# Optimization experiments

Measured on AMD Instinct MI355X. Metric: run time of the kernel, lower is better.

Reference implementation:

```python
import jax, jax.numpy as jnp
import numpy as np

EMBED_DIM = 768
N_HEADS = 12
TIME_RATIO = 0.5
HEAD_DIM = EMBED_DIM // N_HEADS          # 64
T_HEAD = int(HEAD_DIM * TIME_RATIO)      # 32 time dims per head
T_DIM = T_HEAD * N_HEADS                 # 384 time dims overall
EPS = 1e-5


def _ln(v, g, b):
    m = jnp.mean(v, axis=-1, keepdims=True)
    var = jnp.mean((v - m) ** 2, axis=-1, keepdims=True)
    return (v - m) * jax.lax.rsqrt(var + EPS) * g + b


def minkowski_ln(x, g_t, b_t, g_s, b_s):
    # normalize time-like and space-like channel groups separately
    xt, xs = x[..., :T_DIM], x[..., T_DIM:]
    return jnp.concatenate([_ln(xt, g_t, b_t), _ln(xs, g_s, b_s)], axis=-1)


def lorentz_attention(x, Wq, bq, Wk, bk, Wv, bv, Wo, bo):
    B, S, D = x.shape
    def heads(W, b):
        return (x @ W + b).reshape(B, S, N_HEADS, HEAD_DIM).transpose(0, 2, 1, 3)
    q, k, v = heads(Wq, bq), heads(Wk, bk), heads(Wv, bv)
    # Minkowski metric signature (-,...,-,+,...,+) within each head
    eta = jnp.concatenate([-jnp.ones((T_HEAD,), x.dtype), jnp.ones((HEAD_DIM - T_HEAD,), x.dtype)])
    logits = jnp.einsum('bhqd,bhkd->bhqk', q * eta, k) / np.sqrt(HEAD_DIM).astype(np.float32)
    attn = jax.nn.softmax(logits, axis=-1)
    o = jnp.einsum('bhqk,bhkd->bhqd', attn, v)
    o = o.transpose(0, 2, 1, 3).reshape(B, S, D)
    return o @ Wo + bo


def setup_inputs() -> dict:
    key = jax.random.key(0)
    ks = jax.random.split(key, 16)
    D, H4 = EMBED_DIM, EMBED_DIM * 4
    s = 0.02
    inp = {
        'x': jax.random.normal(ks[0], (2, 2048, D), jnp.float32),
        'Wq': jax.random.normal(ks[1], (D, D), jnp.float32) * s, 'bq': jnp.zeros((D,), jnp.float32),
        'Wk': jax.random.normal(ks[2], (D, D), jnp.float32) * s, 'bk': jnp.zeros((D,), jnp.float32),
        'Wv': jax.random.normal(ks[3], (D, D), jnp.float32) * s, 'bv': jnp.zeros((D,), jnp.float32),
        'Wo': jax.random.normal(ks[4], (D, D), jnp.float32) * s, 'bo': jnp.zeros((D,), jnp.float32),
        'g1t': jnp.ones((T_DIM,), jnp.float32), 'b1t': jnp.zeros((T_DIM,), jnp.float32),
        'g1s': jnp.ones((D - T_DIM,), jnp.float32), 'b1s': jnp.zeros((D - T_DIM,), jnp.float32),
        'W1': jax.random.normal(ks[5], (D, H4), jnp.float32) * s, 'bb1': jnp.zeros((H4,), jnp.float32),
        'W2': jax.random.normal(ks[6], (H4, D), jnp.float32) * s, 'bb2': jnp.zeros((D,), jnp.float32),
        'g2t': jnp.ones((T_DIM,), jnp.float32), 'b2t': jnp.zeros((T_DIM,), jnp.float32),
        'g2s': jnp.ones((D - T_DIM,), jnp.float32), 'b2s': jnp.zeros((D - T_DIM,), jnp.float32),
    }
    return inp


def reference(x, Wq, bq, Wk, bk, Wv, bv, Wo, bo,
              g1t, b1t, g1s, b1s, W1, bb1, W2, bb2,
              g2t, b2t, g2s, b2s):
    a = lorentz_attention(x, Wq, bq, Wk, bk, Wv, bv, Wo, bo)
    x = minkowski_ln(x + a, g1t, b1t, g1s, b1s)
    h = jax.nn.gelu(x @ W1 + bb1) @ W2 + bb2
    x = minkowski_ln(x + h, g2t, b2t, g2s, b2s)
    return x
```

## Files before the change

### kernel.cpp

```cpp
#include <hip/hip_runtime.h>
#include <cstddef>
#include <cstdint>

#define D_EMB  768
#define NHEAD  12
#define HDIM   64
#define THEAD  32
#define SEQ    2048
#define BATCH  2
#define NROW   (BATCH*SEQ)
#define HID4   3072

typedef unsigned short u16;
typedef __bf16 bf16x8 __attribute__((ext_vector_type(8)));
typedef float  f32x4  __attribute__((ext_vector_type(4)));
typedef unsigned short u16x8 __attribute__((ext_vector_type(8)));

__device__ __forceinline__ u16 f2bf(float f) {
    unsigned u = __builtin_bit_cast(unsigned, f);
    return (u16)((u + 0x7FFFu + ((u >> 16) & 1u)) >> 16);
}
__device__ __forceinline__ float bf2f(u16 h) {
    return __builtin_bit_cast(float, (unsigned)h << 16);
}

__device__ __forceinline__ void gload_lds16(const void* g, void* l) {
    __builtin_amdgcn_global_load_lds(
        reinterpret_cast<const __attribute__((address_space(1))) void*>(
            reinterpret_cast<uintptr_t>(g)),
        reinterpret_cast<__attribute__((address_space(3))) void*>(
            (uint32_t)reinterpret_cast<uintptr_t>(l)),
        16, 0, 0);
}

__device__ __forceinline__ void tcast(float (*t)[33], const float* __restrict__ W,
                                      u16* __restrict__ WT, int K, int M,
                                      int mt, int kt)
{
    const int m0 = mt * 32, k0 = kt * 32;
    const int tx = threadIdx.x & 31, ty = threadIdx.x >> 5;
#pragma unroll
    for (int i = 0; i < 32; i += 8)
        t[ty + i][tx] = W[(size_t)(k0 + ty + i) * M + m0 + tx];
    __syncthreads();
#pragma unroll
    for (int i = 0; i < 32; i += 8)
        WT[(size_t)(m0 + ty + i) * K + k0 + tx] = f2bf(t[tx][ty + i]);
}

__global__ __launch_bounds__(256)
void prep(const float* __restrict__ Wq, const float* __restrict__ Wk,
          const float* __restrict__ Wv, const float* __restrict__ Wo,
          const float* __restrict__ W1, const float* __restrict__ W2,
          const float* __restrict__ bq, const float* __restrict__ bk,
          const float* __restrict__ bv, const float* __restrict__ x,
          u16* __restrict__ WqkvoT, u16* __restrict__ W1T,
          u16* __restrict__ W2T, u16* __restrict__ xb,
          float* __restrict__ bqkv)
{
    __shared__ float t[32][33];
    const int bid = blockIdx.x;
    if (bid < 2304) {
        const int z = bid / 576, r = bid % 576;
        const float* W = z == 0 ? Wq : z == 1 ? Wk : z == 2 ? Wv : Wo;
        tcast(t, W, WqkvoT + (size_t)z * 768 * 768, 768, 768, r % 24, r / 24);
    } else if (bid < 4608) {
        const int r = bid - 2304;
        tcast(t, W1, W1T, 768, 3072, r % 96, r / 96);
    } else if (bid < 6912) {
        const int r = bid - 4608;
        tcast(t, W2, W2T, 3072, 768, r % 24, r / 24);
    } else if (bid < 8448) {
        const int i = (bid - 6912) * 2048 + threadIdx.x * 8;
        const float4 a = *reinterpret_cast<const float4*>(x + i);
        const float4 b = *reinterpret_cast<const float4*>(x + i + 4);
        u16x8 h;
        h[0] = f2bf(a.x); h[1] = f2bf(a.y); h[2] = f2bf(a.z); h[3] = f2bf(a.w);
        h[4] = f2bf(b.x); h[5] = f2bf(b.y); h[6] = f2bf(b.z); h[7] = f2bf(b.w);
        *reinterpret_cast<u16x8*>(xb + i) = h;
    } else {
        const int i = (bid - 8448) * 256 + threadIdx.x;
        if (i < 2304)
            bqkv[i] = i < 768 ? bq[i] : (i < 1536 ? bk[i - 768] : bv[i - 1536]);
    }
}

template<int EPI>
__global__ __launch_bounds__(256)
void gemm_bf16(const u16* __restrict__ A, const u16* __restrict__ B,
               const float* __restrict__ bias, void* __restrict__ Cp,
               u16* __restrict__ VTp, int K, int N)
{
    __shared__ u16 As[2][128 * 32];
    __shared__ u16 Bs[2][128 * 32];
    const int tid  = threadIdx.x;
    const int lane = tid & 63;
    const int w    = tid >> 6;
    const int m0 = blockIdx.x * 128, n0 = blockIdx.y * 128;
    const int wr = (w >> 1) << 6, wc = (w & 1) << 6;

    const int seg0 = (w << 11) + lane * 16;
    const int row0 = seg0 >> 6, cb0 = (seg0 & 63) >> 1;
    const int seg1 = seg0 + 1024;
    const int row1 = seg1 >> 6, cb1 = (seg1 & 63) >> 1;
    const u16* a0 = A + (size_t)(m0 + row0) * K + cb0;
    const u16* a1 = A + (size_t)(m0 + row1) * K + cb1;
    const u16* b0 = B + (size_t)(n0 + row0) * K + cb0;
    const u16* b1 = B + (size_t)(n0 + row1) * K + cb1;
    const int lo0 = (w * 2 + 0) << 9;
    const int lo1 = (w * 2 + 1) << 9;

    int aIdx[4], bIdx[4];
#pragma unroll
    for (int i = 0; i < 4; ++i) {
        aIdx[i] = (wr + i * 16 + (lane & 15)) * 32 + ((lane >> 4) << 3);
        bIdx[i] = (wc + i * 16 + (lane & 15)) * 32 + ((lane >> 4) << 3);
    }

    f32x4 acc[4][4];
#pragma unroll
    for (int i = 0; i < 4; ++i)
#pragma unroll
        for (int j = 0; j < 4; ++j)
#pragma unroll
            for (int q = 0; q < 4; ++q) acc[i][j][q] = 0.f;

    gload_lds16(a0, &As[0][lo0]);
    gload_lds16(a1, &As[0][lo1]);
    gload_lds16(b0, &Bs[0][lo0]);
    gload_lds16(b1, &Bs[0][lo1]);
    __syncthreads();

    int cur = 0;
    for (int k0 = 0; k0 < K; k0 += 32) {
        if (k0 + 32 < K) {
            gload_lds16(a0 + k0 + 32, &As[cur ^ 1][lo0]);
            gload_lds16(a1 + k0 + 32, &As[cur ^ 1][lo1]);
            gload_lds16(b0 + k0 + 32, &Bs[cur ^ 1][lo0]);
            gload_lds16(b1 + k0 + 32, &Bs[cur ^ 1][lo1]);
        }
        bf16x8 af[4], bv[4];
#pragma unroll
        for (int i = 0; i < 4; ++i)
            af[i] = *reinterpret_cast<const bf16x8*>(&As[cur][aIdx[i]]);
#pragma unroll
        for (int j = 0; j < 4; ++j)
            bv[j] = *reinterpret_cast<const bf16x8*>(&Bs[cur][bIdx[j]]);
#pragma unroll
        for (int i = 0; i < 4; ++i)
#pragma unroll
            for (int j = 0; j < 4; ++j)
                acc[i][j] = __builtin_amdgcn_mfma_f32_16x16x32_bf16(
                    af[i], bv[j], acc[i][j], 0, 0, 0);
        __syncthreads();
        cur ^= 1;
    }

#pragma unroll
    for (int i = 0; i < 4; ++i) {
#pragma unroll
        for (int q = 0; q < 4; ++q) {
            const int row = m0 + wr + i * 16 + ((lane >> 4) << 2) + q;
#pragma unroll
            for (int j = 0; j < 4; ++j) {
                const int col = n0 + wc + j * 16 + (lane & 15);
                float v = acc[i][j][q] + bias[col];
                if (EPI == 2) {
                    const float u3 = v * v * v;
                    v = 0.5f * v * (1.f + tanhf(0.7978845608028654f *
                                                (v + 0.044715f * u3)));
                    ((u16*)Cp)[(size_t)row * N + col] = f2bf(v);
                } else {
                    if (n0 < 1536) {
                        ((u16*)Cp)[(size_t)row * 1536 + col] = f2bf(v);
                    } else {
                        const int c2 = col - 1536;
                        const int hh = c2 >> 6, dd = c2 & 63;
                        const int bb = row >> 11, tok = row & 2047;
                        const int t = tok & 63;
                        const int p = ((t & 15) << 2) | (t >> 4);
                        VTp[((size_t)(bb * NHEAD + hh) * HDIM + dd) * SEQ
                            + (tok & ~63) + p] = f2bf(v);
                    }
                }
            }
        }
    }
}

__global__ __launch_bounds__(256)
void gemm_n64(const u16* __restrict__ A, const u16* __restrict__ B,
              const float* __restrict__ bias, float* __restrict__ C,
              int K, int N)
{
    __shared__ u16 As[2][64 * 32];
    __shared__ u16 Bs[2][128 * 32];
    const int tid  = threadIdx.x;
    const int lane = tid & 63;
    const int w    = tid >> 6;
    const int l15  = lane & 15;
    const int g    = lane >> 4;
    const int m0 = blockIdx.x * 64, n0 = blockIdx.y * 128;

    const int segA = (w << 10) + lane * 16;
    const int rowA = segA >> 6, cbA = (segA & 63) >> 1;
    const u16* aP = A + (size_t)(m0 + rowA) * K + cbA;
    const int loA = w << 9;
    const int seg0 = (w << 11) + lane * 16;
    const int row0 = seg0 >> 6, cb0 = (seg0 & 63) >> 1;
    const int seg1 = seg0 + 1024;
    const int row1 = seg1 >> 6, cb1 = (seg1 & 63) >> 1;
    const u16* b0 = B + (size_t)(n0 + row0) * K + cb0;
    const u16* b1 = B + (size_t)(n0 + row1) * K + cb1;
    const int lo0 = w << 10, lo1 = (w << 10) + 512;

    int aIdx[4], bIdx[2];
#pragma unroll
    for (int i = 0; i < 4; ++i) aIdx[i] = (i * 16 + l15) * 32 + (g << 3);
#pragma unroll
    for (int j = 0; j < 2; ++j) bIdx[j] = ((w << 5) + j * 16 + l15) * 32 + (g << 3);

    f32x4 acc[4][2];
#pragma unroll
    for (int i = 0; i < 4; ++i)
#pragma unroll
        for (int j = 0; j < 2; ++j)
#pragma unroll
            for (int q = 0; q < 4; ++q) acc[i][j][q] = 0.f;

    gload_lds16(aP, &As[0][loA]);
    gload_lds16(b0, &Bs[0][lo0]);
    gload_lds16(b1, &Bs[0][lo1]);
    __syncthreads();

    int cur = 0;
    for (int k0 = 0; k0 < K; k0 += 32) {
        if (k0 + 32 < K) {
            gload_lds16(aP + k0 + 32, &As[cur ^ 1][loA]);
            gload_lds16(b0 + k0 + 32, &Bs[cur ^ 1][lo0]);
            gload_lds16(b1 + k0 + 32, &Bs[cur ^ 1][lo1]);
        }
        bf16x8 af[4], bv[2];
#pragma unroll
        for (int i = 0; i < 4; ++i)
            af[i] = *reinterpret_cast<const bf16x8*>(&As[cur][aIdx[i]]);
#pragma unroll
        for (int j = 0; j < 2; ++j)
            bv[j] = *reinterpret_cast<const bf16x8*>(&Bs[cur][bIdx[j]]);
#pragma unroll
        for (int i = 0; i < 4; ++i)
#pragma unroll
            for (int j = 0; j < 2; ++j)
                acc[i][j] = __builtin_amdgcn_mfma_f32_16x16x32_bf16(
                    af[i], bv[j], acc[i][j], 0, 0, 0);
        __syncthreads();
        cur ^= 1;
    }

#pragma unroll
    for (int i = 0; i < 4; ++i) {
#pragma unroll
        for (int q = 0; q < 4; ++q) {
            const int row = m0 + i * 16 + (g << 2) + q;
#pragma unroll
            for (int j = 0; j < 2; ++j) {
                const int col = n0 + (w << 5) + j * 16 + l15;
                C[(size_t)row * N + col] = acc[i][j][q] + bias[col];
            }
        }
    }
}

#define SM_SCALE 0.18033688011112042f

__global__ __launch_bounds__(256)
void attn_mfma(const u16* __restrict__ QK, const u16* __restrict__ VT,
               u16* __restrict__ O)
{
    __shared__ u16 Ks[2][64 * 64];
    __shared__ u16 Vs[2][64 * 64];
    __shared__ u16 Ps[64 * 72];

    const int tid  = threadIdx.x;
    const int lane = tid & 63;
    const int w    = tid >> 6;
    const int l15  = lane & 15;
    const int g    = lane >> 4;
    const int bh   = blockIdx.x;
    const int b    = bh / NHEAD, h = bh % NHEAD;
    const int q0   = blockIdx.y * 64;
    const int bS   = b * SEQ;

    bf16x8 aq[2];
    {
        const u16* Qg = QK + (size_t)(bS + q0 + (w << 4) + l15) * 1536 + h * HDIM;
#pragma unroll
        for (int kk = 0; kk < 2; ++kk) {
            const u16x8 hq = *reinterpret_cast<const u16x8*>(Qg + kk * 32 + g * 8);
            const float sc = (kk == 0) ? -SM_SCALE : SM_SCALE;
            u16x8 hs;
#pragma unroll
            for (int j = 0; j < 8; ++j)
                hs[j] = __builtin_bit_cast(u16, (__bf16)(bf2f(hq[j]) * sc));
            aq[kk] = __builtin_bit_cast(bf16x8, hs);
        }
    }

    const int rl = lane >> 3;
    const int cs = ((lane & 7) ^ rl) << 3;
    const u16* pK = QK + (size_t)(bS + 16 * w + rl) * 1536 + 768 + h * HDIM + cs;
    const u16* pV = VT + ((size_t)(b * NHEAD + h) * HDIM + 16 * w + rl) * SEQ + cs;

    int swz[2];
#pragma unroll
    for (int kk = 0; kk < 2; ++kk)
        swz[kk] = ((kk * 4 + g) ^ (l15 & 7)) << 3;

    bf16x8 vones;
    {
        u16x8 o16;
#pragma unroll
        for (int j = 0; j < 8; ++j) o16[j] = 0x3F80u;
        vones = __builtin_bit_cast(bf16x8, o16);
    }

    f32x4 accO[4];
#pragma unroll
    for (int n = 0; n < 4; ++n)
#pragma unroll
        for (int q = 0; q < 4; ++q) accO[n][q] = 0.f;
    f32x4 accS;
#pragma unroll
    for (int q = 0; q < 4; ++q) accS[q] = 0.f;

#define ATTN_STAGE(c, kt)                                                   \
    do {                                                                    \
        u16* dK = &Ks[c][w * 1024];                                         \
        u16* dV = &Vs[c][w * 1024];                                         \
        gload_lds16(pK + (size_t)(kt) * 1536,       dK);                    \
        gload_lds16(pK + (size_t)((kt) + 8) * 1536, dK + 512);              \
        gload_lds16(pV + (kt),           dV);                               \
        gload_lds16(pV + (kt) + 8 * SEQ, dV + 512);                         \
    } while (0)

    ATTN_STAGE(0, 0);
    __syncthreads();
    int cur = 0;

    for (int kt = 0; kt < SEQ; kt += 64) {
        if (kt + 64 < SEQ) ATTN_STAGE(cur ^ 1, kt + 64);

        f32x4 sac[4];
#pragma unroll
        for (int n = 0; n < 4; ++n) {
#pragma unroll
            for (int q = 0; q < 4; ++q) sac[n][q] = 0.f;
#pragma unroll
            for (int kk = 0; kk < 2; ++kk) {
                const bf16x8 bk = *reinterpret_cast<const bf16x8*>(
                    &Ks[cur][(n * 16 + l15) * 64 + swz[kk]]);
                sac[n] = __builtin_amdgcn_mfma_f32_16x16x32_bf16(
                    aq[kk], bk, sac[n], 0, 0, 0);
            }
        }

#pragma unroll
        for (int r4 = 0; r4 < 4; ++r4) {
            const int prow = (w << 4) + (g << 2) + r4;
            const float sv0 = __builtin_amdgcn_exp2f(sac[0][r4]);
            const float sv1 = __builtin_amdgcn_exp2f(sac[1][r4]);
            const float sv2 = __builtin_amdgcn_exp2f(sac[2][r4]);
            const float sv3 = __builtin_amdgcn_exp2f(sac[3][r4]);
            ushort4 pk4;
            pk4.x = __builtin_bit_cast(u16, (__bf16)sv0);
            pk4.y = __builtin_bit_cast(u16, (__bf16)sv1);
            pk4.z = __builtin_bit_cast(u16, (__bf16)sv2);
            pk4.w = __builtin_bit_cast(u16, (__bf16)sv3);
            *reinterpret_cast<ushort4*>(&Ps[prow * 72 + (l15 << 2)]) = pk4;
        }

        bf16x8 pa[2];
#pragma unroll
        for (int kk = 0; kk < 2; ++kk)
            pa[kk] = *reinterpret_cast<const bf16x8*>(
                &Ps[((w << 4) + l15) * 72 + kk * 32 + g * 8]);
#pragma unroll
        for (int n = 0; n < 4; ++n) {
#pragma unroll
            for (int kk = 0; kk < 2; ++kk) {
                const bf16x8 bv = *reinterpret_cast<const bf16x8*>(
                    &Vs[cur][(n * 16 + l15) * 64 + swz[kk]]);
                accO[n] = __builtin_amdgcn_mfma_f32_16x16x32_bf16(
                    pa[kk], bv, accO[n], 0, 0, 0);
            }
        }
#pragma unroll
        for (int kk = 0; kk < 2; ++kk)
            accS = __builtin_amdgcn_mfma_f32_16x16x32_bf16(
                pa[kk], vones, accS, 0, 0, 0);
        __syncthreads();
        cur ^= 1;
    }

#pragma unroll
    for (int r4 = 0; r4 < 4; ++r4) {
        const float inv = 1.f / accS[r4];
        const int qr = q0 + (w << 4) + (g << 2) + r4;
#pragma unroll
        for (int n = 0; n < 4; ++n)
            O[(size_t)(bS + qr) * D_EMB + h * HDIM + n * 16 + l15]
                = f2bf(accO[n][r4] * inv);
    }
#undef ATTN_STAGE
}

__global__ __launch_bounds__(256)
void mink_ln(const float* __restrict__ X, const float* __restrict__ R,
             const float* __restrict__ gt, const float* __restrict__ bt,
             const float* __restrict__ gs, const float* __restrict__ bs,
             float* __restrict__ Out, u16* __restrict__ OutB, int nrows)
{
    const int wid  = (int)((blockIdx.x * 256 + threadIdx.x) >> 6);
    const int lane = threadIdx.x & 63;
    const int row  = wid >> 1, half = wid & 1;
    if (row >= nrows) return;

    const float* g  = half ? gs : gt;
    const float* bb = half ? bs : bt;
    const size_t base = (size_t)row * D_EMB + half * 384;

    float v[6];
    float sum = 0.f;
#pragma unroll
    for (int i = 0; i < 6; ++i) {
        const float t = X[base + i * 64 + lane] + R[base + i * 64 + lane];
        v[i] = t; sum += t;
    }
#pragma unroll
    for (int off = 32; off; off >>= 1) sum += __shfl_xor(sum, off);
    const float mean = sum * (1.f / 384.f);

    float ss = 0.f;
#pragma unroll
    for (int i = 0; i < 6; ++i) { const float d = v[i] - mean; ss += d * d; }
#pragma unroll
    for (int off = 32; off; off >>= 1) ss += __shfl_xor(ss, off);
    const float rstd = rsqrtf(ss * (1.f / 384.f) + 1e-5f);

#pragma unroll
    for (int i = 0; i < 6; ++i) {
        const int e = i * 64 + lane;
        const float o = (v[i] - mean) * rstd * g[e] + bb[e];
        Out[base + e] = o;
        if (OutB) OutB[base + e] = f2bf(o);
    }
}

extern "C" void kernel_launch(void* const* d_in, const int* in_sizes, int n_in,
                              void* d_out, int out_size, void* d_ws, size_t ws_size,
                              hipStream_t stream)
{
    const float* x   = (const float*)d_in[0];
    const float* Wq  = (const float*)d_in[1];
    const float* bq  = (const float*)d_in[2];
    const float* Wk  = (const float*)d_in[3];
    const float* bk  = (const float*)d_in[4];
    const float* Wv  = (const float*)d_in[5];
    const float* bv  = (const float*)d_in[6];
    const float* Wo  = (const float*)d_in[7];
    const float* bo  = (const float*)d_in[8];
    const float* g1t = (const float*)d_in[9];
    const float* b1t = (const float*)d_in[10];
    const float* g1s = (const float*)d_in[11];
    const float* b1s = (const float*)d_in[12];
    const float* W1  = (const float*)d_in[13];
    const float* bb1 = (const float*)d_in[14];
    const float* W2  = (const float*)d_in[15];
    const float* bb2 = (const float*)d_in[16];
    const float* g2t = (const float*)d_in[17];
    const float* b2t = (const float*)d_in[18];
    const float* g2s = (const float*)d_in[19];
    const float* b2s = (const float*)d_in[20];
    float* out = (float*)d_out;

    const size_t ND = (size_t)NROW * D_EMB;
    u16* WqkvoT = (u16*)d_ws;
    u16* W1T = WqkvoT + 2359296;
    u16* W2T = W1T + 2359296;
    u16* xb  = W2T + 2359296;
    u16* QKb = xb + ND;
    u16* VTb = QKb + (size_t)NROW * 1536;
    u16* Ab  = VTb + ND;
    u16* Hb  = QKb;
    float* AoF  = (float*)(Ab + ND);
    float* bqkv = AoF;
    float* X1   = AoF + ND;

    const dim3 blk(256);

    prep<<<8457, blk, 0, stream>>>(Wq, Wk, Wv, Wo, W1, W2, bq, bk, bv, x,
                                   WqkvoT, W1T, W2T, xb, bqkv);

    gemm_bf16<3><<<dim3(32, 18), blk, 0, stream>>>(xb, WqkvoT, bqkv, QKb, VTb,
                                                   768, 2304);
    attn_mfma<<<dim3(BATCH * NHEAD, SEQ / 64), blk, 0, stream>>>(QKb, VTb, Ab);

    gemm_n64<<<dim3(64, 6), blk, 0, stream>>>(Ab, WqkvoT + (size_t)2304 * 768,
                                              bo, AoF, 768, 768);
    mink_ln<<<2048, blk, 0, stream>>>(x, AoF, g1t, b1t, g1s, b1s, X1, xb, NROW);
    gemm_bf16<2><<<dim3(32, 24), blk, 0, stream>>>(xb, W1T, bb1, Hb, nullptr,
                                                   768, 3072);
    gemm_n64<<<dim3(64, 6), blk, 0, stream>>>(Hb, W2T, bb2, AoF, 3072, 768);
    mink_ln<<<2048, blk, 0, stream>>>(X1, AoF, g2t, b2t, g2s, b2s, out, nullptr, NROW);
}
```

Measured before the change: 195.1 us.

## Split-K the N=768 GEMMs in two and fold partial sums into LayerNorm

The two output-projection GEMMs (attention out and MLP down) now run with a 2-way split-K over blockIdx.z, doubling the grid from 384 to 768 blocks. The second partial sum is written to a separate fp32 buffer (reusing the QK scratch or the output buffer), and the Minkowski LayerNorm kernels add both partials. The aim is better CU occupancy on a small grid, at the cost of extra fp32 writes and reads. The second LN reads and writes `out` in place, which is safe per element.

```diff
diff --git a/kernel.cpp b/kernel.cpp
--- a/kernel.cpp
+++ b/kernel.cpp
@@ -190,8 +190,8 @@
 
 __global__ __launch_bounds__(256)
 void gemm_n64(const u16* __restrict__ A, const u16* __restrict__ B,
-              const float* __restrict__ bias, float* __restrict__ C,
-              int K, int N)
+              const float* __restrict__ bias, float* __restrict__ C0,
+              float* __restrict__ C1, int Khalf, int Ktot, int N)
 {
     __shared__ u16 As[2][64 * 32];
     __shared__ u16 Bs[2][128 * 32];
@@ -201,17 +201,20 @@
     const int l15  = lane & 15;
     const int g    = lane >> 4;
     const int m0 = blockIdx.x * 64, n0 = blockIdx.y * 128;
+    const int zz = blockIdx.z;
+    const int kbase = zz * Khalf;
+    float* __restrict__ C = zz ? C1 : C0;
 
     const int segA = (w << 10) + lane * 16;
     const int rowA = segA >> 6, cbA = (segA & 63) >> 1;
-    const u16* aP = A + (size_t)(m0 + rowA) * K + cbA;
+    const u16* aP = A + (size_t)(m0 + rowA) * Ktot + kbase + cbA;
     const int loA = w << 9;
     const int seg0 = (w << 11) + lane * 16;
     const int row0 = seg0 >> 6, cb0 = (seg0 & 63) >> 1;
     const int seg1 = seg0 + 1024;
     const int row1 = seg1 >> 6, cb1 = (seg1 & 63) >> 1;
-    const u16* b0 = B + (size_t)(n0 + row0) * K + cb0;
-    const u16* b1 = B + (size_t)(n0 + row1) * K + cb1;
+    const u16* b0 = B + (size_t)(n0 + row0) * Ktot + kbase + cb0;
+    const u16* b1 = B + (size_t)(n0 + row1) * Ktot + kbase + cb1;
     const int lo0 = w << 10, lo1 = (w << 10) + 512;
 
     int aIdx[4], bIdx[2];
@@ -234,8 +237,8 @@
     __syncthreads();
 
     int cur = 0;
-    for (int k0 = 0; k0 < K; k0 += 32) {
-        if (k0 + 32 < K) {
+    for (int k0 = 0; k0 < Khalf; k0 += 32) {
+        if (k0 + 32 < Khalf) {
             gload_lds16(aP + k0 + 32, &As[cur ^ 1][loA]);
             gload_lds16(b0 + k0 + 32, &Bs[cur ^ 1][lo0]);
             gload_lds16(b1 + k0 + 32, &Bs[cur ^ 1][lo1]);
@@ -265,7 +268,8 @@
 #pragma unroll
             for (int j = 0; j < 2; ++j) {
                 const int col = n0 + (w << 5) + j * 16 + l15;
-                C[(size_t)row * N + col] = acc[i][j][q] + bias[col];
+                const float bb = zz ? 0.f : bias[col];
+                C[(size_t)row * N + col] = acc[i][j][q] + bb;
             }
         }
     }
@@ -415,7 +419,8 @@
 }
 
 __global__ __launch_bounds__(256)
-void mink_ln(const float* __restrict__ X, const float* __restrict__ R,
+void mink_ln(const float* __restrict__ X, const float* __restrict__ R1,
+             const float* __restrict__ R2,
              const float* __restrict__ gt, const float* __restrict__ bt,
              const float* __restrict__ gs, const float* __restrict__ bs,
              float* __restrict__ Out, u16* __restrict__ OutB, int nrows)
@@ -433,7 +438,8 @@
     float sum = 0.f;
 #pragma unroll
     for (int i = 0; i < 6; ++i) {
-        const float t = X[base + i * 64 + lane] + R[base + i * 64 + lane];
+        const size_t e = base + i * 64 + lane;
+        const float t = X[e] + R1[e] + R2[e];
         v[i] = t; sum += t;
     }
 #pragma unroll
@@ -492,6 +498,7 @@
     u16* VTb = QKb + (size_t)NROW * 1536;
     u16* Ab  = VTb + ND;
     u16* Hb  = QKb;
+    float* QKf  = (float*)QKb;
     float* AoF  = (float*)(Ab + ND);
     float* bqkv = AoF;
     float* X1   = AoF + ND;
@@ -505,11 +512,14 @@
                                                    768, 2304);
     attn_mfma<<<dim3(BATCH * NHEAD, SEQ / 64), blk, 0, stream>>>(QKb, VTb, Ab);
 
-    gemm_n64<<<dim3(64, 6), blk, 0, stream>>>(Ab, WqkvoT + (size_t)2304 * 768,
-                                              bo, AoF, 768, 768);
-    mink_ln<<<2048, blk, 0, stream>>>(x, AoF, g1t, b1t, g1s, b1s, X1, xb, NROW);
+    gemm_n64<<<dim3(64, 6, 2), blk, 0, stream>>>(
+        Ab, WqkvoT + (size_t)2304 * 768, bo, AoF, QKf, 384, 768, 768);
+    mink_ln<<<2048, blk, 0, stream>>>(x, AoF, QKf, g1t, b1t, g1s, b1s,
+                                      X1, xb, NROW);
     gemm_bf16<2><<<dim3(32, 24), blk, 0, stream>>>(xb, W1T, bb1, Hb, nullptr,
                                                    768, 3072);
-    gemm_n64<<<dim3(64, 6), blk, 0, stream>>>(Hb, W2T, bb2, AoF, 3072, 768);
-    mink_ln<<<2048, blk, 0, stream>>>(X1, AoF, g2t, b2t, g2s, b2s, out, nullptr, NROW);
-}
+    gemm_n64<<<dim3(64, 6, 2), blk, 0, stream>>>(
+        Hb, W2T, bb2, AoF, out, 1536, 3072, 768);
+    mink_ln<<<2048, blk, 0, stream>>>(X1, AoF, out, g2t, b2t, g2s, b2s,
+                                      out, nullptr, NROW);
+}
```

Result: faster. 191.0 us (-2.1%).
